# Kernel optimization log

Measured on AMD Instinct MI355X. Metric: run time of the kernel, lower is better.

Reference implementation:

```python
import jax, jax.numpy as jnp
import numpy as np

N_QUBITS = 12
BATCH = 2048
N_CLASSES = 10


def build_tape(n):
    # 2 layers of: RX on all wires (id 0), RY (id 1), RZ (id 2), then a CRX ring
    # (id 4 forward in layer 0, id 5 reversed in layer 1). 96 gates total for n=12.
    tape = []
    for layer in range(2):
        for i in range(n):
            tape.append(("rx", (i,)))
        for i in range(n):
            tape.append(("ry", (i,)))
        for i in range(n):
            tape.append(("rz", (i,)))
        order = range(n) if layer == 0 else range(n - 1, -1, -1)
        for i in order:
            tape.append(("crx", (i, (i + 1) % n)))
    return tape


def rx_mat(t):
    c = jnp.cos(t / 2).astype(jnp.complex64)
    s = jnp.sin(t / 2).astype(jnp.complex64)
    return jnp.stack([jnp.stack([c, -1j * s]), jnp.stack([-1j * s, c])])


def ry_mat(t):
    c = jnp.cos(t / 2).astype(jnp.complex64)
    s = jnp.sin(t / 2).astype(jnp.complex64)
    return jnp.stack([jnp.stack([c, -s]), jnp.stack([s, c])])


def rz_mat(t):
    em = jnp.exp(-1j * t.astype(jnp.complex64) / 2)
    ep = jnp.exp(1j * t.astype(jnp.complex64) / 2)
    z = jnp.zeros((), jnp.complex64)
    return jnp.stack([jnp.stack([em, z]), jnp.stack([z, ep])])


def apply_1q(psi, U, w):
    # psi: [B] + [2]*n, gate on wire w (axis 1+w)
    psi = jnp.moveaxis(psi, 1 + w, -1)
    psi = psi @ U.T
    return jnp.moveaxis(psi, -1, 1 + w)


def apply_crx(psi, theta, c, t):
    a_c, a_t = 1 + c, 1 + t
    psi = jnp.moveaxis(psi, a_c, 1)  # control -> axis 1
    if a_t < a_c:
        a_t += 1
    psi = jnp.moveaxis(psi, a_t, -1)  # target -> last axis
    U = rx_mat(theta)
    p1 = psi[:, 1] @ U.T  # apply RX only on control=1 branch
    psi = jnp.stack([psi[:, 0], p1], axis=1)
    psi = jnp.moveaxis(psi, -1, a_t)
    return jnp.moveaxis(psi, 1, a_c)


def expvals(psi, n):
    # <X_i>, <Y_i>, <Z_i> for each qubit; returns [B, 3n] ordered X..Y..Z (PL order)
    xs, ys, zs = [], [], []
    for i in range(n):
        p = jnp.moveaxis(psi, 1 + i, -1).reshape(psi.shape[0], -1, 2)
        z = jnp.sum(jnp.abs(p[..., 0]) ** 2 - jnp.abs(p[..., 1]) ** 2, axis=1)
        cross = jnp.sum(jnp.conj(p[..., 0]) * p[..., 1], axis=1)
        xs.append(2.0 * jnp.real(cross))
        ys.append(2.0 * jnp.imag(cross))
        zs.append(jnp.real(z))
    return jnp.stack(xs + ys + zs, axis=1).astype(jnp.float32)


def setup_inputs() -> dict:
    key = jax.random.key(0)
    k0, k1, k2 = jax.random.split(key, 3)
    sv = jax.random.normal(k0, (BATCH, 2 ** N_QUBITS), dtype=jnp.float32)
    sv = sv / jnp.linalg.norm(sv, axis=1, keepdims=True)  # valid quantum states
    n_gates = len(build_tape(N_QUBITS))
    angles = jax.random.normal(k1, (n_gates,), dtype=jnp.float32)
    W = jax.random.normal(k2, (N_CLASSES, 3 * N_QUBITS), dtype=jnp.float32) * 0.1
    b = jnp.zeros((N_CLASSES,), jnp.float32)
    return {"state_vectors": sv, "angles": angles, "W": W, "b": b}


def reference(state_vectors, angles, W, b):
    tape = build_tape(N_QUBITS)
    psi = state_vectors.astype(jnp.complex64).reshape((-1,) + (2,) * N_QUBITS)
    for g, (kind, wires) in enumerate(tape):
        th = angles[g]
        if kind == "rx":
            psi = apply_1q(psi, rx_mat(th), wires[0])
        elif kind == "ry":
            psi = apply_1q(psi, ry_mat(th), wires[0])
        elif kind == "rz":
            psi = apply_1q(psi, rz_mat(th), wires[0])
        else:
            psi = apply_crx(psi, th, wires[0], wires[1])
    feats = expvals(psi, N_QUBITS)  # [B, 3*n_qubits]
    return feats @ W.T + b
```

## Files before the change

kernel.cpp:

```cpp
#include <hip/hip_runtime.h>

#define DIM 4096
using F2 = float2;


__device__ __forceinline__ int caddrA (int r, int t) { return ((r >> 1) << 6) | t; }
__device__ __forceinline__ int caddrB1(int r, int t) { return ((t >> 1) << 6) | (r & 62) | (t & 1); }
__device__ __forceinline__ int caddrB2(int r, int t) {
    return ((t >> 1) << 6) | ((r & 1) << 5) | (((r >> 4) & 3) << 3)
         | (((r >> 1) & 3) << 1) | (t & 1);
}
__device__ __forceinline__ int caddrC2(int r, int t) {
    return (((r >> 1) & 1) << 10) | ((r & 1) << 9) | (t << 3)
         | (((r >> 5) & 1) << 2) | (((r >> 4) & 1) << 1) | ((r >> 2) & 1);
}
__device__ __forceinline__ int swz(int a) { return a ^ ((a >> 6) & 15); }

__device__ __forceinline__ F2 pk_mul_bl(F2 a, F2 u) {
    F2 d;
    asm("v_pk_mul_f32 %0, %1, %2 op_sel:[0,0] op_sel_hi:[1,0]"
        : "=v"(d) : "v"(a), "v"(u));
    return d;
}
__device__ __forceinline__ void pk_cross(F2& d, F2 a, F2 u) {
    asm("v_pk_fma_f32 %0, %1, %2, %0 op_sel:[1,1,0] op_sel_hi:[0,1,1] neg_lo:[1,0,0]"
        : "+v"(d) : "v"(a), "v"(u));
}
__device__ __forceinline__ void pk_fma_bl(F2& d, F2 a, F2 u) {
    asm("v_pk_fma_f32 %0, %1, %2, %0 op_sel:[0,0,0] op_sel_hi:[1,0,1]"
        : "+v"(d) : "v"(a), "v"(u));
}
__device__ __forceinline__ void pk_swapneg(F2& d, F2 a, F2 cs) {
    asm("v_pk_fma_f32 %0, %1, %2, %0 op_sel:[1,1,0] op_sel_hi:[0,1,1] neg_hi:[1,0,0]"
        : "+v"(d) : "v"(a), "v"(cs));
}
__device__ __forceinline__ void pk_fma(F2& d, F2 a, F2 b) {
    asm("v_pk_fma_f32 %0, %1, %2, %0" : "+v"(d) : "v"(a), "v"(b));
}
__device__ __forceinline__ void pk_imacc(F2& d, F2 a0, F2 a1) {
    asm("v_pk_fma_f32 %0, %1, %2, %0 op_sel:[0,1,0] op_sel_hi:[1,0,1] neg_hi:[1,0,0]"
        : "+v"(d) : "v"(a0), "v"(a1));
}
__device__ __forceinline__ F2 pk_cmul(F2 u, F2 a) {
    F2 d = pk_mul_bl(a, u);
    pk_cross(d, a, u);
    return d;
}
__device__ __forceinline__ void pk_cfma(F2& d, F2 u, F2 a) {
    pk_fma_bl(d, a, u);
    pk_cross(d, a, u);
}

__device__ __forceinline__ void build_u(float tx, float ty, float tz, float* u) {
    float sx = sinf(0.5f*tx), cx = cosf(0.5f*tx);
    float sy = sinf(0.5f*ty), cy = cosf(0.5f*ty);
    float sz = sinf(0.5f*tz), cz = cosf(0.5f*tz);
    float A00r = cy*cx, A00i =  sy*sx;
    float A01r = -sy*cx, A01i = -cy*sx;
    float A10r =  sy*cx, A10i = -cy*sx;
    float A11r =  cy*cx, A11i = -sy*sx;
    u[0] = cz*A00r + sz*A00i;  u[1] = cz*A00i - sz*A00r;
    u[2] = cz*A01r + sz*A01i;  u[3] = cz*A01i - sz*A01r;
    u[4] = cz*A10r - sz*A10i;  u[5] = cz*A10i + sz*A10r;
    u[6] = cz*A11r - sz*A11i;  u[7] = cz*A11i + sz*A11r;
}

__global__ void prep_kernel(const float* __restrict__ ang, float* __restrict__ coef) {
    int t = threadIdx.x;
    if (t < 12) {
        float u[8]; build_u(ang[t], ang[12+t], ang[24+t], u);
#pragma unroll
        for (int j = 0; j < 8; ++j) coef[t*8 + j] = u[j];
    } else if (t < 24) {
        int q = t - 12;
        float u[8]; build_u(ang[48+q], ang[60+q], ang[72+q], u);
#pragma unroll
        for (int j = 0; j < 8; ++j) coef[192 + q*8 + j] = u[j];
    } else if (t < 36) {
        int c = t - 24;
        float th = 0.5f * ang[95 - c];
        coef[296 + c*2]     = cosf(th);
        coef[296 + c*2 + 1] = sinf(th);
    } else if (t < 47) {
        int q = t - 35;
        float u[8]; build_u(ang[q], ang[12+q], ang[24+q], u);
        float c = cosf(0.5f*ang[36+q-1]), s = sinf(0.5f*ang[36+q-1]);
        float m[8];
        m[0] = c*u[0] + s*u[5];  m[1] = c*u[1] - s*u[4];
        m[2] = c*u[2] + s*u[7];  m[3] = c*u[3] - s*u[6];
        m[4] = s*u[1] + c*u[4];  m[5] = -s*u[0] + c*u[5];
        m[6] = s*u[3] + c*u[6];  m[7] = -s*u[2] + c*u[7];
#pragma unroll
        for (int j = 0; j < 8; ++j) coef[96 + q*8 + j] = m[j];
    } else if (t == 47) {
        float u[8]; build_u(ang[48], ang[60], ang[72], u);
        float c = cosf(0.5f*ang[47]), s = sinf(0.5f*ang[47]);
        float m[8];
        m[0] = c*u[0] + s*u[3];  m[1] = c*u[1] - s*u[2];
        m[2] = s*u[1] + c*u[2];  m[3] = -s*u[0] + c*u[3];
        m[4] = c*u[4] + s*u[7];  m[5] = c*u[5] - s*u[6];
        m[6] = s*u[5] + c*u[6];  m[7] = -s*u[4] + c*u[7];
#pragma unroll
        for (int j = 0; j < 8; ++j) coef[288 + j] = m[j];
    }
}

template<int M, int SB, int HB>
__device__ __forceinline__ void g1q(F2* amp, const float* __restrict__ u) {
    F2 u00 = {u[0], u[1]}, u01 = {u[2], u[3]};
    F2 u10 = {u[4], u[5]}, u11 = {u[6], u[7]};
#pragma unroll
    for (int r0 = 0; r0 < 64; ++r0) {
        if (r0 & M) continue;
        if (SB != 0 && (r0 & SB) != HB) continue;
        const int r1 = r0 + M;
        F2 a0 = amp[r0], a1 = amp[r1];
        F2 n0 = pk_cmul(u00, a0); pk_cfma(n0, u01, a1);
        F2 n1 = pk_cmul(u10, a0); pk_cfma(n1, u11, a1);
        amp[r0] = n0; amp[r1] = n1;
    }
}

template<int MSEL, int M, int SB, int HB>
__device__ __forceinline__ void fg1q(F2* amp, const float* __restrict__ uA,
                                     const float* __restrict__ uB) {
    F2 a00 = {uA[0], uA[1]}, a01 = {uA[2], uA[3]}, a10 = {uA[4], uA[5]}, a11 = {uA[6], uA[7]};
    F2 b00 = {uB[0], uB[1]}, b01 = {uB[2], uB[3]}, b10 = {uB[4], uB[5]}, b11 = {uB[6], uB[7]};
#pragma unroll
    for (int r0 = 0; r0 < 64; ++r0) {
        if (r0 & M) continue;
        if (SB != 0 && (r0 & SB) != HB) continue;
        const int r1 = r0 + M;
        const bool sel = (r0 & MSEL) != 0;
        F2 u00 = sel ? b00 : a00, u01 = sel ? b01 : a01;
        F2 u10 = sel ? b10 : a10, u11 = sel ? b11 : a11;
        F2 a0 = amp[r0], a1 = amp[r1];
        F2 n0 = pk_cmul(u00, a0); pk_cfma(n0, u01, a1);
        F2 n1 = pk_cmul(u10, a0); pk_cfma(n1, u11, a1);
        amp[r0] = n0; amp[r1] = n1;
    }
}

template<int MC, int MT>
__device__ __forceinline__ void crx(F2* amp, F2 cs) {
#pragma unroll
    for (int r0 = 0; r0 < 64; ++r0) {
        if (!(r0 & MC) || (r0 & MT)) continue;
        const int r1 = r0 + MT;
        F2 a0 = amp[r0], a1 = amp[r1];
        F2 n0 = pk_mul_bl(a0, cs); pk_swapneg(n0, a1, cs);
        F2 n1 = pk_mul_bl(a1, cs); pk_swapneg(n1, a0, cs);
        amp[r0] = n0; amp[r1] = n1;
    }
}

template<int M>
__device__ __forceinline__ void expv(const F2* amp, int q, int lane,
                                     float& fx, float& fy, float& fz) {
    F2 zp = {0.f, 0.f}, zm = {0.f, 0.f}, xp = {0.f, 0.f}, ip = {0.f, 0.f};
#pragma unroll
    for (int r0 = 0; r0 < 64; ++r0) {
        if (r0 & M) continue;
        const int r1 = r0 + M;
        F2 a0 = amp[r0], a1 = amp[r1];
        pk_fma(zp, a0, a0);
        pk_fma(zm, a1, a1);
        pk_fma(xp, a0, a1);
        pk_imacc(ip, a0, a1);
    }
    float zz = (zp.x + zp.y) - (zm.x + zm.y);
    float xr = 2.f * (xp.x + xp.y);
    float xi = 2.f * (ip.x + ip.y);
#pragma unroll
    for (int off = 32; off; off >>= 1) {
        xr += __shfl_xor(xr, off);
        xi += __shfl_xor(xi, off);
        zz += __shfl_xor(zz, off);
    }
    if (lane == q) { fx = xr; fy = xi; fz = zz; }
}

template<int M, int SB>
__device__ __forceinline__ int r0_of(int j, int hb) {
    int r = hb ? SB : 0, b = 1;
#pragma unroll
    for (int p = 0; p < 6; ++p) {
        const int mm = 1 << p;
        if (mm == M || mm == SB) continue;
        if (j & b) r |= mm;
        b <<= 1;
    }
    return r;
}

#define ST_H(CADDR, SB, HB) \
  { _Pragma("unroll") for (int r = 0; r < 64; ++r) { \
      if ((r & (SB)) != (HB)) continue; \
      psi[swz(CADDR(r, t))] = amp[r]; } }
#define LD_H(CADDR, M, SB, HB) \
  { _Pragma("unroll") for (int k = 0; k < 32; ++k) { \
      const int j = k >> 1; \
      const int r0 = r0_of<M, SB>(j, (HB) != 0); \
      const int r = (k & 1) ? (r0 + (M)) : r0; \
      amp[r] = psi[swz(CADDR(r, t))]; } }

#define U0P(q, M)               g1q<M, 0, 0>(amp, cf + (q)*8)
#define FU0(q, MS, M)           fg1q<MS, M, 0, 0>(amp, cf + (q)*8, cf + 96 + (q)*8)
#define FU0_H(q, MS, M, SB, HB) fg1q<MS, M, SB, HB>(amp, cf + (q)*8, cf + 96 + (q)*8)
#define U1P(q, M)               g1q<M, 0, 0>(amp, cf + 192 + (q)*8)
#define U1P_H(q, M, SB, HB)     g1q<M, SB, HB>(amp, cf + 192 + (q)*8)
#define FU1_0()                 fg1q<4, 2, 0, 0>(amp, cf + 192, cf + 288)
#define CR1(c, MC, MT)          crx<MC, MT>(amp, F2{cf[296 + (c)*2], cf[296 + (c)*2 + 1]})
#define EXPV(q, M)              expv<M>(amp, q, t, fx, fy, fz)

__global__ __launch_bounds__(64, 1)
void qsim_kernel(const float* __restrict__ sv,
                 const float* __restrict__ cf,
                 const float* __restrict__ W,
                 const float* __restrict__ bvec,
                 float* __restrict__ out)
{
    __shared__ F2 psi[2048];
    const int t = threadIdx.x;
    const int b = blockIdx.x;

    F2 amp[64];
    const float* svb = sv + (size_t)b * DIM;
#pragma unroll
    for (int k = 0; k < 64; ++k) {
        const int r = (k & 1) ? ((k >> 1) + 32) : (k >> 1);
        amp[r] = make_float2(svb[(r << 6) | t], 0.f);
    }

    float fx = 0.f, fy = 0.f, fz = 0.f;

    U0P(0, 32);
    FU0(1, 32, 16); FU0(2, 16, 8); FU0(3, 8, 4); FU0(4, 4, 2); FU0(5, 2, 1);

    ST_H(caddrA, 1, 0);
    __syncthreads();
    LD_H(caddrB1, 32, 1, 0);
    __syncthreads();
    ST_H(caddrA, 1, 1);
    FU0_H(6, 1, 32, 1, 0);
    __syncthreads();
    LD_H(caddrB1, 32, 1, 1);
    FU0_H(6, 1, 32, 1, 1);

    FU0(7, 32, 16); FU0(8, 16, 8); FU0(9, 8, 4); FU0(10, 4, 2);

    __syncthreads();
    ST_H(caddrB2, 8, 0);
    __syncthreads();
    LD_H(caddrC2, 4, 8, 0);
    __syncthreads();
    ST_H(caddrB2, 8, 8);
    FU0_H(11, 16, 4, 8, 0);
    __syncthreads();
    LD_H(caddrC2, 4, 8, 8);
    FU0_H(11, 16, 4, 8, 8);

    FU1_0();
    U1P(1, 1); U1P(8, 8); U1P(9, 32); U1P(10, 16); U1P(11, 4);
    CR1(11, 4, 2); CR1(10, 16, 4); CR1(9, 32, 16); CR1(8, 8, 32);

    __syncthreads();
    ST_H(caddrC2, 8, 0);
    EXPV(9, 32); EXPV(10, 16); EXPV(11, 4);
    __syncthreads();
    LD_H(caddrB2, 1, 8, 0);
    __syncthreads();
    ST_H(caddrC2, 8, 8);
    U1P_H(5, 1, 8, 0);
    __syncthreads();
    LD_H(caddrB2, 1, 8, 8);
    U1P_H(5, 1, 8, 8);

    U1P(6, 32); U1P(7, 16);
    CR1(7, 16, 8); CR1(6, 32, 16); CR1(5, 1, 32);

    __syncthreads();
    ST_H(caddrB1, 1, 0);
    EXPV(6, 32); EXPV(7, 16); EXPV(8, 8);
    __syncthreads();
    LD_H(caddrA, 8, 1, 0);
    __syncthreads();
    ST_H(caddrB1, 1, 1);
    U1P_H(2, 8, 1, 0);
    __syncthreads();
    LD_H(caddrA, 8, 1, 1);
    U1P_H(2, 8, 1, 1);

    U1P(3, 4); U1P(4, 2);
    CR1(4, 2, 1); CR1(3, 4, 2); CR1(2, 8, 4); CR1(1, 16, 8); CR1(0, 32, 16);
    EXPV(0, 32); EXPV(1, 16); EXPV(2, 8); EXPV(3, 4); EXPV(4, 2); EXPV(5, 1);

    __syncthreads();
    float* fbuf = (float*)psi;
    if (t < 12) {
        fbuf[t]      = fx;
        fbuf[12 + t] = fy;
        fbuf[24 + t] = fz;
    }
    __syncthreads();
    if (t < 10) {
        float a = bvec[t];
#pragma unroll
        for (int f = 0; f < 36; ++f)
            a += W[t * 36 + f] * fbuf[f];
        out[(size_t)b * 10 + t] = a;
    }
}

extern "C" void kernel_launch(void* const* d_in, const int* in_sizes, int n_in,
                              void* d_out, int out_size, void* d_ws, size_t ws_size,
                              hipStream_t stream) {
    const float* sv     = (const float*)d_in[0];
    const float* angles = (const float*)d_in[1];
    const float* W      = (const float*)d_in[2];
    const float* bvec   = (const float*)d_in[3];
    float* out  = (float*)d_out;
    float* coef = (float*)d_ws;
    int batch = in_sizes[0] / DIM;
    prep_kernel<<<1, 64, 0, stream>>>(angles, coef);
    qsim_kernel<<<batch, 64, 0, stream>>>(sv, coef, W, bvec, out);
}
```

Before: 148.6 us.

## Split each state vector across four waves with 16 amplitudes per thread

Each block now runs 256 threads instead of 64, so every thread holds 16 amplitudes rather than 64. The qubit-to-register/lane/wave mapping and the shared-memory transpose layouts are redesigned so most exchanges stay within one wave and need only an LDS waitcnt fence; block-wide barriers are used only when a wave-index qubit must move. Expectation values are reduced per wave and summed across the four waves before the final linear layer. The aim is less register pressure and higher occupancy. The cost is more complex XOR-swizzled addressing and some extra block barriers.

```diff
diff --git a/kernel.cpp b/kernel.cpp
--- a/kernel.cpp
+++ b/kernel.cpp
@@ -3,18 +3,6 @@
 #define DIM 4096
 using F2 = float2;
 
-
-__device__ __forceinline__ int caddrA (int r, int t) { return ((r >> 1) << 6) | t; }
-__device__ __forceinline__ int caddrB1(int r, int t) { return ((t >> 1) << 6) | (r & 62) | (t & 1); }
-__device__ __forceinline__ int caddrB2(int r, int t) {
-    return ((t >> 1) << 6) | ((r & 1) << 5) | (((r >> 4) & 3) << 3)
-         | (((r >> 1) & 3) << 1) | (t & 1);
-}
-__device__ __forceinline__ int caddrC2(int r, int t) {
-    return (((r >> 1) & 1) << 10) | ((r & 1) << 9) | (t << 3)
-         | (((r >> 5) & 1) << 2) | (((r >> 4) & 1) << 1) | ((r >> 2) & 1);
-}
-__device__ __forceinline__ int swz(int a) { return a ^ ((a >> 6) & 15); }
 
 __device__ __forceinline__ F2 pk_mul_bl(F2 a, F2 u) {
     F2 d;
@@ -105,12 +93,45 @@
     }
 }
 
+__device__ __forceinline__ int rpA1(int r) {
+    int a11=(r>>3)&1, a10=(r>>2)&1, a9=(r>>1)&1;
+    return (a11<<8)|(a10<<7)|(a9<<6)|(a11<<3)|(a10<<2)|(a9<<1)|(a9<<0);
+}
+__device__ __forceinline__ int rpB1(int r) {
+    int a5=(r>>1)&1, a7=(r>>2)&1, a6=(r>>3)&1;
+    return (a7<<5)|(a6<<4)|(a7<<3)|(a6<<2)|(a5<<0);
+}
+__device__ __forceinline__ int rpB2(int r) {
+    int a8=r&1, a7=(r>>2)&1, a6=(r>>3)&1;
+    return (a8<<5)|(a7<<4)|(a6<<3)|(a7<<2)|(a8<<1)|(a6<<0);
+}
+__device__ __forceinline__ int rpC2(int r) {
+    int a2=r&1, a4=(r>>2)&1, a3=(r>>3)&1;
+    return (a3<<3)|(a2<<2)|(a4<<1);
+}
+__device__ __forceinline__ int rpC3(int r) {
+    int a5=(r>>1)&1, a4=(r>>2)&1, a3=(r>>3)&1;
+    return (a5<<4)|(a3<<3)|(a4<<2)|(a5<<0);
+}
+__device__ __forceinline__ int rpD3(int r) {
+    int a1=(r>>1)&1, a0=(r>>2)&1, a11=(r>>3)&1;
+    return (a11<<8)|(a11<<3)|(a1<<1)|((a0^a11)<<0);
+}
+__device__ __forceinline__ int rpC5(int r) {
+    int a2=r&1, a4=(r>>2)&1, a3=(r>>3)&1;
+    return (a4<<4)|(a3<<3)|(a2<<2)|(a4<<0);
+}
+__device__ __forceinline__ int rpB5(int r) {
+    int a8=r&1, a7=(r>>2)&1, a6=(r>>3)&1;
+    return (a7<<10)|(a6<<9)|(a8<<5)|(a8<<3);
+}
+
 template<int M, int SB, int HB>
 __device__ __forceinline__ void g1q(F2* amp, const float* __restrict__ u) {
     F2 u00 = {u[0], u[1]}, u01 = {u[2], u[3]};
     F2 u10 = {u[4], u[5]}, u11 = {u[6], u[7]};
 #pragma unroll
-    for (int r0 = 0; r0 < 64; ++r0) {
+    for (int r0 = 0; r0 < 16; ++r0) {
         if (r0 & M) continue;
         if (SB != 0 && (r0 & SB) != HB) continue;
         const int r1 = r0 + M;
@@ -127,7 +148,7 @@
     F2 a00 = {uA[0], uA[1]}, a01 = {uA[2], uA[3]}, a10 = {uA[4], uA[5]}, a11 = {uA[6], uA[7]};
     F2 b00 = {uB[0], uB[1]}, b01 = {uB[2], uB[3]}, b10 = {uB[4], uB[5]}, b11 = {uB[6], uB[7]};
 #pragma unroll
-    for (int r0 = 0; r0 < 64; ++r0) {
+    for (int r0 = 0; r0 < 16; ++r0) {
         if (r0 & M) continue;
         if (SB != 0 && (r0 & SB) != HB) continue;
         const int r1 = r0 + M;
@@ -144,7 +165,7 @@
 template<int MC, int MT>
 __device__ __forceinline__ void crx(F2* amp, F2 cs) {
 #pragma unroll
-    for (int r0 = 0; r0 < 64; ++r0) {
+    for (int r0 = 0; r0 < 16; ++r0) {
         if (!(r0 & MC) || (r0 & MT)) continue;
         const int r1 = r0 + MT;
         F2 a0 = amp[r0], a1 = amp[r1];
@@ -159,7 +180,7 @@
                                      float& fx, float& fy, float& fz) {
     F2 zp = {0.f, 0.f}, zm = {0.f, 0.f}, xp = {0.f, 0.f}, ip = {0.f, 0.f};
 #pragma unroll
-    for (int r0 = 0; r0 < 64; ++r0) {
+    for (int r0 = 0; r0 < 16; ++r0) {
         if (r0 & M) continue;
         const int r1 = r0 + M;
         F2 a0 = amp[r0], a1 = amp[r1];
@@ -184,7 +205,7 @@
 __device__ __forceinline__ int r0_of(int j, int hb) {
     int r = hb ? SB : 0, b = 1;
 #pragma unroll
-    for (int p = 0; p < 6; ++p) {
+    for (int p = 0; p < 4; ++p) {
         const int mm = 1 << p;
         if (mm == M || mm == SB) continue;
         if (j & b) r |= mm;
@@ -193,27 +214,29 @@
     return r;
 }
 
-#define ST_H(CADDR, SB, HB) \
-  { _Pragma("unroll") for (int r = 0; r < 64; ++r) { \
+#define ST_T(TP, RP, SB, HB) \
+  { _Pragma("unroll") for (int r = 0; r < 16; ++r) { \
       if ((r & (SB)) != (HB)) continue; \
-      psi[swz(CADDR(r, t))] = amp[r]; } }
-#define LD_H(CADDR, M, SB, HB) \
-  { _Pragma("unroll") for (int k = 0; k < 32; ++k) { \
+      psi[(TP) ^ RP(r)] = amp[r]; } }
+#define LD_T(TP, RP, M, SB, HB) \
+  { _Pragma("unroll") for (int k = 0; k < 8; ++k) { \
       const int j = k >> 1; \
       const int r0 = r0_of<M, SB>(j, (HB) != 0); \
       const int r = (k & 1) ? (r0 + (M)) : r0; \
-      amp[r] = psi[swz(CADDR(r, t))]; } }
+      amp[r] = psi[(TP) ^ RP(r)]; } }
+
+#define WAVE_FENCE asm volatile("s_waitcnt lgkmcnt(0)" ::: "memory")
 
 #define U0P(q, M)               g1q<M, 0, 0>(amp, cf + (q)*8)
 #define FU0(q, MS, M)           fg1q<MS, M, 0, 0>(amp, cf + (q)*8, cf + 96 + (q)*8)
 #define FU0_H(q, MS, M, SB, HB) fg1q<MS, M, SB, HB>(amp, cf + (q)*8, cf + 96 + (q)*8)
 #define U1P(q, M)               g1q<M, 0, 0>(amp, cf + 192 + (q)*8)
 #define U1P_H(q, M, SB, HB)     g1q<M, SB, HB>(amp, cf + 192 + (q)*8)
-#define FU1_0()                 fg1q<4, 2, 0, 0>(amp, cf + 192, cf + 288)
+#define FU1_0()                 fg1q<4, 8, 0, 0>(amp, cf + 192, cf + 288)
 #define CR1(c, MC, MT)          crx<MC, MT>(amp, F2{cf[296 + (c)*2], cf[296 + (c)*2 + 1]})
-#define EXPV(q, M)              expv<M>(amp, q, t, fx, fy, fz)
-
-__global__ __launch_bounds__(64, 1)
+#define EXPV(q, M)              expv<M>(amp, q, l, fx, fy, fz)
+
+__global__ __launch_bounds__(256, 6)
 void qsim_kernel(const float* __restrict__ sv,
                  const float* __restrict__ cf,
                  const float* __restrict__ W,
@@ -223,91 +246,131 @@
     __shared__ F2 psi[2048];
     const int t = threadIdx.x;
     const int b = blockIdx.x;
-
-    F2 amp[64];
+    const int l = t & 63, w = t >> 6;
+    const int w1 = (w >> 1) & 1, w0 = w & 1;
+    const int l0 = l & 1, l1 = (l >> 1) & 1, l2 = (l >> 2) & 1;
+    const int l3 = (l >> 3) & 1, l4 = (l >> 4) & 1, l5 = (l >> 5) & 1;
+
+    F2 amp[16];
     const float* svb = sv + (size_t)b * DIM;
 #pragma unroll
-    for (int k = 0; k < 64; ++k) {
-        const int r = (k & 1) ? ((k >> 1) + 32) : (k >> 1);
-        amp[r] = make_float2(svb[(r << 6) | t], 0.f);
+    for (int k = 0; k < 16; ++k) {
+        const int r = (k & 1) ? ((k >> 1) + 8) : (k >> 1);
+        amp[r] = make_float2(svb[(r << 8) | (l << 2) | w], 0.f);
     }
 
     float fx = 0.f, fy = 0.f, fz = 0.f;
 
-    U0P(0, 32);
-    FU0(1, 32, 16); FU0(2, 16, 8); FU0(3, 8, 4); FU0(4, 4, 2); FU0(5, 2, 1);
-
-    ST_H(caddrA, 1, 0);
+    U0P(0, 8);
+    FU0(1, 8, 4); FU0(2, 4, 2); FU0(3, 2, 1);
+
+    {
+        const int tpA = (w1<<10)|(w0<<9)|(l5<<5)|(l4<<4)|((l1^l5)<<3)|((l0^l4)<<2)|(l2<<1)|(l3<<0);
+        const int tpB = (w1<<10)|(w0<<9)|(l5<<8)|(l4<<7)|(l3<<6)|((l1^l5)<<3)|((l0^l4)<<2)|((l2^l3)<<1)|(l3<<0);
+        ST_T(tpA, rpA1, 1, 0); WAVE_FENCE;
+        LD_T(tpB, rpB1, 4, 1, 0); WAVE_FENCE;
+        ST_T(tpA, rpA1, 1, 1);
+        FU0_H(4, 1, 4, 1, 0);
+        WAVE_FENCE;
+        LD_T(tpB, rpB1, 4, 1, 1);
+        FU0_H(4, 1, 4, 1, 1);
+    }
+    FU0(5, 4, 8); FU0(6, 8, 2);
+
+    {
+        const int tpB = (w1<<10)|(w0<<9)|(l5<<8)|(l4<<7)|(l3<<6)|((l1^l5)<<3)|((l0^l4)<<2)|((l2^l3)<<1)|(l3<<0);
+        const int tpC = (w1<<10)|(w0<<9)|(l5<<8)|(l4<<7)|(l3<<6)|(l2<<5)|(l1<<4)|((l5^l0)<<3)|((l4^l1)<<2)|((l3^l2)<<1)|((l0^l3)<<0);
+        ST_T(tpB, rpB2, 2, 0); WAVE_FENCE;
+        LD_T(tpC, rpC2, 4, 2, 0); WAVE_FENCE;
+        ST_T(tpB, rpB2, 2, 2);
+        FU0_H(7, 2, 4, 2, 0);
+        WAVE_FENCE;
+        LD_T(tpC, rpC2, 4, 2, 2);
+        FU0_H(7, 2, 4, 2, 2);
+    }
+    FU0(8, 4, 8); FU0(9, 8, 1);
+
     __syncthreads();
-    LD_H(caddrB1, 32, 1, 0);
-    __syncthreads();
-    ST_H(caddrA, 1, 1);
-    FU0_H(6, 1, 32, 1, 0);
-    __syncthreads();
-    LD_H(caddrB1, 32, 1, 1);
-    FU0_H(6, 1, 32, 1, 1);
-
-    FU0(7, 32, 16); FU0(8, 16, 8); FU0(9, 8, 4); FU0(10, 4, 2);
-
-    __syncthreads();
-    ST_H(caddrB2, 8, 0);
-    __syncthreads();
-    LD_H(caddrC2, 4, 8, 0);
-    __syncthreads();
-    ST_H(caddrB2, 8, 8);
-    FU0_H(11, 16, 4, 8, 0);
-    __syncthreads();
-    LD_H(caddrC2, 4, 8, 8);
-    FU0_H(11, 16, 4, 8, 8);
-
+    {
+        const int tpC = (l1<<10)|(l0<<9)|(l5<<8)|(l4<<7)|(l3<<6)|(l2<<5)|((l5^l4)<<3)|(l3<<2)|((w1^l2)<<1)|((w0^l5)<<0);
+        const int tpD = (w1<<10)|(w0<<9)|(l5<<7)|(l4<<6)|(l3<<5)|(l2<<4)|((l0^l5)<<3)|((l1^l4)<<2)|(l3<<1)|(l2<<0);
+        ST_T(tpC, rpC3, 1, 0);
+        __syncthreads();
+        LD_T(tpD, rpD3, 2, 1, 0);
+        __syncthreads();
+        ST_T(tpC, rpC3, 1, 1);
+        FU0_H(10, 1, 2, 1, 0);
+        __syncthreads();
+        LD_T(tpD, rpD3, 2, 1, 1);
+        FU0_H(10, 1, 2, 1, 1);
+    }
+    FU0(11, 2, 4);
     FU1_0();
-    U1P(1, 1); U1P(8, 8); U1P(9, 32); U1P(10, 16); U1P(11, 4);
-    CR1(11, 4, 2); CR1(10, 16, 4); CR1(9, 32, 16); CR1(8, 8, 32);
-
-    __syncthreads();
-    ST_H(caddrC2, 8, 0);
-    EXPV(9, 32); EXPV(10, 16); EXPV(11, 4);
-    __syncthreads();
-    LD_H(caddrB2, 1, 8, 0);
-    __syncthreads();
-    ST_H(caddrC2, 8, 8);
-    U1P_H(5, 1, 8, 0);
-    __syncthreads();
-    LD_H(caddrB2, 1, 8, 8);
-    U1P_H(5, 1, 8, 8);
-
-    U1P(6, 32); U1P(7, 16);
-    CR1(7, 16, 8); CR1(6, 32, 16); CR1(5, 1, 32);
-
-    __syncthreads();
-    ST_H(caddrB1, 1, 0);
-    EXPV(6, 32); EXPV(7, 16); EXPV(8, 8);
-    __syncthreads();
-    LD_H(caddrA, 8, 1, 0);
-    __syncthreads();
-    ST_H(caddrB1, 1, 1);
-    U1P_H(2, 8, 1, 0);
-    __syncthreads();
-    LD_H(caddrA, 8, 1, 1);
-    U1P_H(2, 8, 1, 1);
-
-    U1P(3, 4); U1P(4, 2);
-    CR1(4, 2, 1); CR1(3, 4, 2); CR1(2, 8, 4); CR1(1, 16, 8); CR1(0, 32, 16);
-    EXPV(0, 32); EXPV(1, 16); EXPV(2, 8); EXPV(3, 4); EXPV(4, 2); EXPV(5, 1);
+    U1P(9, 1); U1P(10, 2); U1P(11, 4);
+    CR1(11, 4, 8); CR1(10, 2, 4); CR1(9, 1, 2);
+    EXPV(10, 2); EXPV(11, 4);
+
+    {
+        const int tpD = (w1<<10)|(w0<<9)|(l5<<7)|(l4<<6)|(l3<<5)|(l2<<4)|((l0^l5)<<3)|((l1^l4)<<2)|(l3<<1)|(l2<<0);
+        const int tpC = (w1<<10)|(w0<<9)|(l5<<8)|(l4<<7)|(l3<<6)|(l2<<5)|((l5^l4)<<3)|(l3<<2)|((l1^l2)<<1)|((l0^l5)<<0);
+        ST_T(tpD, rpD3, 1, 0); WAVE_FENCE;
+        LD_T(tpC, rpC3, 4, 1, 0); WAVE_FENCE;
+        ST_T(tpD, rpD3, 1, 1);
+        U1P_H(7, 4, 1, 0);
+        WAVE_FENCE;
+        LD_T(tpC, rpC3, 4, 1, 1);
+        U1P_H(7, 4, 1, 1);
+    }
+    U1P(6, 2); U1P(8, 8);
+    CR1(8, 8, 1); CR1(7, 4, 8); CR1(6, 2, 4);
+    EXPV(9, 1); EXPV(8, 8); EXPV(7, 4);
+
+    {
+        const int tpC = (w1<<10)|(w0<<9)|(l5<<8)|(l4<<7)|(l3<<6)|(l2<<5)|((l5^l2)<<3)|(l4<<2)|((l1^l3)<<1)|(l0<<0);
+        const int tpB = (l5<<8)|(l4<<7)|(l3<<6)|(l2<<4)|((l1^l5)<<3)|((l0^l4)<<2)|((w1^l3)<<1)|((w0^l2)<<0);
+        ST_T(tpC, rpC5, 2, 0);
+        __syncthreads();
+        LD_T(tpB, rpB5, 1, 2, 0);
+        __syncthreads();
+        ST_T(tpC, rpC5, 2, 2);
+        U1P_H(3, 1, 2, 0);
+        __syncthreads();
+        LD_T(tpB, rpB5, 1, 2, 2);
+        U1P_H(3, 1, 2, 2);
+        __syncthreads();
+    }
+    U1P(4, 4); U1P(5, 8);
+    CR1(5, 8, 2); CR1(4, 4, 8); CR1(3, 1, 4);
+    EXPV(6, 2); EXPV(5, 8); EXPV(4, 4);
+
+    {
+        const int tpB = (w1<<10)|(w0<<9)|(l5<<8)|(l4<<7)|(l3<<6)|((l1^l5)<<3)|((l0^l4)<<2)|((l2^l3)<<1)|(l3<<0);
+        const int tpA = (w1<<10)|(w0<<9)|(l5<<5)|(l4<<4)|((l1^l5)<<3)|((l0^l4)<<2)|(l2<<1)|(l3<<0);
+        ST_T(tpB, rpB1, 1, 0); WAVE_FENCE;
+        LD_T(tpA, rpA1, 4, 1, 0); WAVE_FENCE;
+        ST_T(tpB, rpB1, 1, 1);
+        U1P_H(1, 4, 1, 0);
+        WAVE_FENCE;
+        LD_T(tpA, rpA1, 4, 1, 1);
+        U1P_H(1, 4, 1, 1);
+    }
+    U1P(2, 2);
+    CR1(2, 2, 1); CR1(1, 4, 2); CR1(0, 8, 4);
+    EXPV(3, 1); EXPV(2, 2); EXPV(1, 4); EXPV(0, 8);
 
     __syncthreads();
     float* fbuf = (float*)psi;
-    if (t < 12) {
-        fbuf[t]      = fx;
-        fbuf[12 + t] = fy;
-        fbuf[24 + t] = fz;
+    if (l < 12) {
+        fbuf[w * 36 + l]      = fx;
+        fbuf[w * 36 + 12 + l] = fy;
+        fbuf[w * 36 + 24 + l] = fz;
     }
     __syncthreads();
     if (t < 10) {
         float a = bvec[t];
 #pragma unroll
         for (int f = 0; f < 36; ++f)
-            a += W[t * 36 + f] * fbuf[f];
+            a += W[t * 36 + f] * (fbuf[f] + fbuf[36 + f] + fbuf[72 + f] + fbuf[108 + f]);
         out[(size_t)b * 10 + t] = a;
     }
 }
@@ -323,5 +386,5 @@
     float* coef = (float*)d_ws;
     int batch = in_sizes[0] / DIM;
     prep_kernel<<<1, 64, 0, stream>>>(angles, coef);
-    qsim_kernel<<<batch, 64, 0, stream>>>(sv, coef, W, bvec, out);
-}
+    qsim_kernel<<<batch, 256, 0, stream>>>(sv, coef, W, bvec, out);
+}
```

After: 155.3 us. 4.5% more time.
